# Kernel optimization log

Hardware: AMD Instinct MI355X
Metric: run time of the kernel (lower is better)

Reference implementation:

```python
import jax, jax.numpy as jnp
import numpy as np
import math

LOG_2PI = math.log(2.0 * math.pi)
MIN_CLIP, MAX_CLIP = -5.0, 5.0


def _lse(x, axis):
    return jax.nn.logsumexp(x, axis=axis)


def _gaussian_multi(m1, v1, m2, v2):
    # product of two diagonal Gaussians in log-std parameterization
    v1s = jnp.exp(2.0 * v1)
    v2s = jnp.exp(2.0 * v2)
    add = v1s + v2s
    la = jnp.log(add)
    scale = (-0.5 * (LOG_2PI + la + (m1 - m2) ** 2 / add)).sum(-1)
    mu = (m1 * v2s + m2 * v1s) / add
    var = v1 + v2 - 0.5 * la
    return scale, mu, var


def _energy(sents, mask, tw, tpm, tpv, tcm, tcv, sw_tab, sm_tab, sv_tab):
    B, T = sents.shape
    L, _, TC = tw.shape
    G = tpm.shape[-1]
    EC = sw_tab.shape[1] // L
    clip = lambda x: jnp.clip(x, MIN_CLIP, MAX_CLIP)
    s_mu = clip(sm_tab[sents].reshape(B, T, 1, L, 1, EC, G))
    s_var = clip(sv_tab[sents].reshape(B, T, 1, L, 1, EC, G))
    s_w = sw_tab[sents].reshape(B, T, 1, L, 1, EC)
    t_w = tw.reshape(1, 1, 1, L, L, 1, 1, TC)
    t_p_mu = clip(tpm.reshape(1, 1, 1, L, L, 1, 1, TC, G))
    t_p_var = clip(tpv.reshape(1, 1, 1, L, L, 1, 1, TC, G))
    t_c_mu = clip(tcm.reshape(1, 1, L, L, TC, 1, G))
    t_c_var = clip(tcv.reshape(1, 1, L, L, TC, 1, G))
    cs_scale, cs_mu, cs_var = _gaussian_multi(s_mu, s_var, t_c_mu, t_c_var)
    cs_scale = cs_scale + s_w  # (B,T,L,L,TC,EC)
    # parent-child fusion over consecutive timesteps -> (B,T-1,L,L,L,TC,EC,TC)
    csp, _, _ = _gaussian_multi(jnp.expand_dims(cs_mu[:, :-1], (4, 7)),
                                jnp.expand_dims(cs_var[:, :-1], (4, 7)),
                                t_p_mu, t_p_var)
    mask1 = mask[:, 1:].reshape(B, T - 1, 1, 1, 1, 1, 1, 1)
    csp = csp * mask1 + jnp.expand_dims(cs_scale[:, :-1], (4, 7)) + t_w * mask1
    last = jnp.broadcast_to(jnp.expand_dims(cs_scale[:, -1:], (4, 7)),
                            (B, 1, L, L, L, TC, EC, TC))
    energy = jnp.concatenate([csp, last], axis=1)
    return energy * mask.reshape(B, T, 1, 1, 1, 1, 1, 1)


def _loss(sents, target, mask, tw, tpm, tpv, tcm, tcv, sw_tab, sm_tab, sv_tab):
    B, T = sents.shape
    L, _, TC = tw.shape
    energy = _energy(sents, mask, tw, tpm, tpv, tcm, tcv, sw_tab, sm_tab, sv_tab)
    e_t = jnp.moveaxis(energy, 1, 0)  # (T,B,L,L,L,TC,EC,TC)
    tgt_t = target.T                  # (T,B)
    tgt_next = jnp.concatenate([tgt_t[1:], jnp.zeros((1, B), tgt_t.dtype)], axis=0)
    mask_t = mask.T                   # (T,B)
    bidx = jnp.arange(B)
    # t = 0 : root label is L-1
    e0 = e_t[0]
    part = _lse(_lse(e0[:, -1], axis=4), axis=3)  # (B,L,L,TC)
    tmp0 = e0[bidx, jnp.full((B,), L - 1), tgt_t[0], tgt_next[0]]  # (B,TC,EC,TC)
    tgt_e = _lse(_lse(tmp0, axis=2), axis=1)      # (B,TC) (initial tgt_energy is zeros)

    def step(carry, xs):
        part, tgt_e = carry
        e, tg, tn, pv, m = xs
        pn = _lse(_lse(_lse(e + part[:, :, :, None, :, None, None], 5), 4), 1)
        part = part + (pn - part) * m[:, None, None, None]
        tmp = e[bidx, pv, tg, tn]  # (B,TC,EC,TC)
        te_new = _lse(_lse(tmp + tgt_e[:, :, None, None], 2), 1)
        tgt_e = tgt_e + (te_new - tgt_e) * m[:, None]
        return (part, tgt_e), None

    (part, tgt_e), _ = jax.lax.scan(
        step, (part, tgt_e),
        (e_t[1:], tgt_t[1:], tgt_next[1:], tgt_t[:-1], mask_t[1:]))
    part = part.mean(axis=2)  # (B,L,TC)
    loss = _lse(_lse(part, 2), 1) - _lse(tgt_e, 1)
    return loss.mean()


def setup_inputs() -> dict:
    key = jax.random.key(0)
    ks = jax.random.split(key, 10)
    V, NL, G, TC, EC = 50000, 45, 1, 1, 1
    L = NL + 1
    B, T = 4, 96

    def xavier(k, shape):
        rf = int(np.prod(shape[2:])) if len(shape) > 2 else 1
        fan_in = shape[1] * rf
        fan_out = shape[0] * rf
        std = math.sqrt(2.0 / (fan_in + fan_out))
        return jax.random.normal(k, shape, jnp.float32) * std

    return {
        "sents": jax.random.randint(ks[0], (B, T), 0, V, dtype=jnp.int32),
        "target": jax.random.randint(ks[1], (B, T), 0, NL, dtype=jnp.int32),
        "mask": jnp.ones((B, T), jnp.float32),
        "trans_weight": xavier(ks[2], (L, L, TC)),
        "trans_p_mu": xavier(ks[3], (L, L, TC, G)),
        "trans_p_var": xavier(ks[4], (L, L, TC, G)),
        "trans_c_mu": xavier(ks[5], (L, L, TC, G)),
        "trans_c_var": xavier(ks[6], (L, L, TC, G)),
        "s_weight_tab": jax.random.normal(ks[7], (V, L * EC), jnp.float32),
        "s_mu_tab": jax.random.normal(ks[8], (V, L * G * EC), jnp.float32),
        "s_var_tab": jax.random.normal(ks[9], (V, L * G * EC), jnp.float32),
    }


def reference(sents, target, mask, trans_weight, trans_p_mu, trans_p_var,
              trans_c_mu, trans_c_var, s_weight_tab, s_mu_tab, s_var_tab):
    return _loss(sents, target, mask, trans_weight, trans_p_mu, trans_p_var,
                 trans_c_mu, trans_c_var, s_weight_tab, s_mu_tab, s_var_tab)
```

## Files before the change

kernel.cpp:

```cpp
#include <hip/hip_runtime.h>
#include <hip/hip_fp16.h>
#include <math.h>

#define L 46
#define LSQ 2116
#define T 96
#define B 4
#define WROWF 52
#define KSTRIDE_U32 25600
#define LOG_2PI 1.8378770664093453f
#define LN2f 0.6931471805599453f

typedef float v2f __attribute__((ext_vector_type(2)));

__device__ __forceinline__ float clip5(float x) {
    return fminf(fmaxf(x, -5.0f), 5.0f);
}

__device__ __forceinline__ unsigned fxform(float f) {
    unsigned u = __float_as_uint(f);
    return (u & 0x80000000u) ? ~u : (u | 0x80000000u);
}
__device__ __forceinline__ float funxform(unsigned u) {
    return __uint_as_float((u & 0x80000000u) ? (u ^ 0x80000000u) : ~u);
}

#define BARRIER_LGKM() asm volatile("s_waitcnt lgkmcnt(0)\n\ts_barrier" ::: "memory")

__device__ __forceinline__ unsigned enc_e4m3_sw(float f) {
    if (!(f >= 0.0f)) return 0u;
    if (f < 0.015625f) {
        int m = (int)rintf(f * 512.0f);
        return (unsigned)m;
    }
    unsigned u = __float_as_uint(fminf(f, 448.0f));
    int e = (int)((u >> 23) & 255) - 127;
    int mant = (int)((u >> 20) & 7) + (int)((u >> 19) & 1);
    int Eb = e + 7;
    if (mant == 8) { mant = 0; ++Eb; }
    if (Eb > 15) { Eb = 15; mant = 6; }
    return (unsigned)((Eb << 3) | mant);
}
template <bool HI>
__device__ __forceinline__ unsigned enc_pk(float a, float b, unsigned old) {
#if __has_builtin(__builtin_amdgcn_cvt_pk_fp8_f32)
    return (unsigned)__builtin_amdgcn_cvt_pk_fp8_f32(a, b, (int)old, HI);
#else
    unsigned lo = enc_e4m3_sw(a) | (enc_e4m3_sw(b) << 8);
    return HI ? ((old & 0x0000FFFFu) | (lo << 16)) : ((old & 0xFFFF0000u) | lo);
#endif
}

__device__ __forceinline__ float dec1_sw(unsigned b) {
    int e = (b >> 3) & 15, m = b & 7;
    return e ? ldexpf((float)(8 + m), e - 10) : ldexpf((float)m, -9);
}
template <bool HI>
__device__ __forceinline__ v2f dec_pk(unsigned u) {
#if __has_builtin(__builtin_amdgcn_cvt_pk_f32_fp8)
    return __builtin_amdgcn_cvt_pk_f32_fp8(u, HI);
#else
    unsigned x = HI ? (u >> 16) : u;
    v2f r; r.x = dec1_sw(x & 0xffu); r.y = dec1_sw((x >> 8) & 0xffu);
    return r;
#endif
}

__device__ __forceinline__ void dp_acc(v2f& acc, unsigned kv, v2f wA, v2f wB) {
    acc += dec_pk<false>(kv) * wA;
    acc += dec_pk<true>(kv)  * wB;
}

__global__ __launch_bounds__(1024) void build_kernel(
    const int*   __restrict__ sents,
    const int*   __restrict__ target,
    const float* __restrict__ tw,
    const float* __restrict__ tpm,
    const float* __restrict__ tpv,
    const float* __restrict__ tcm,
    const float* __restrict__ tcv,
    const float* __restrict__ sw_tab,
    const float* __restrict__ sm_tab,
    const float* __restrict__ sv_tab,
    unsigned* __restrict__ K8,
    float*    __restrict__ escB,
    float*    __restrict__ psD,
    float*    __restrict__ P0,
    float*    __restrict__ tgtc,
    unsigned* __restrict__ done)
{
    __shared__ float sPS[LSQ], sMU[LSQ], sW1[LSQ], sW2[LSQ], sTP[LSQ];
    const int bt = blockIdx.x;
    const int t  = bt % T;
    const int b  = bt / T;
    const int sent = sents[bt];

    if (bt == 0 && threadIdx.x == 0) *done = 0u;

    for (int i = threadIdx.x; i < LSQ; i += 1024) {
        sW2[i] = __expf(2.0f * clip5(tpv[i]));
        sTP[i] = clip5(tpm[i]);
        int bb = i % L;
        float smu  = clip5(sm_tab[sent * L + bb]);
        float svar = clip5(sv_tab[sent * L + bb]);
        float sw   = sw_tab[sent * L + bb];
        float tc_m = clip5(tcm[i]);
        float tc_v = clip5(tcv[i]);
        float v1s = __expf(2.0f * svar);
        float v2s = __expf(2.0f * tc_v);
        float add = v1s + v2s;
        float inv = __builtin_amdgcn_rcpf(add);
        float la  = __logf(add);
        float d   = smu - tc_m;
        float psv = fmaf(-0.5f, LOG_2PI + la + d * d * inv, sw);
        sPS[i] = psv;
        psD[(size_t)bt * LSQ + i] = psv;
        sMU[i] = (smu * v2s + tc_m * v1s) * inv;
        sW1[i] = v1s * v2s * inv;
    }
    __syncthreads();

    if (threadIdx.x == 0) {
        const int* tg = target + b * T;
        float contrib;
        if (t == 0) {
            int i1 = 45 * L + tg[0], i2 = tg[0] * L + tg[1];
            float ad = sW1[i1] + sW2[i2];
            float d  = sMU[i1] - sTP[i2];
            contrib = sPS[i1] + tw[i2]
                    - 0.5f * (LOG_2PI + __logf(ad) + d * d * __builtin_amdgcn_rcpf(ad));
        } else if (t == T - 1) {
            contrib = sPS[tg[T - 2] * L + tg[T - 1]];
        } else {
            int i1 = tg[t - 1] * L + tg[t], i2 = tg[t] * L + tg[t + 1];
            float ad = sW1[i1] + sW2[i2];
            float d  = sMU[i1] - sTP[i2];
            contrib = sPS[i1] + tw[i2]
                    - 0.5f * (LOG_2PI + __logf(ad) + d * d * __builtin_amdgcn_rcpf(ad));
        }
        tgtc[bt] = contrib;
    }

    if (t == 0) {
        for (int oi = threadIdx.x; oi < LSQ; oi += 1024) {
            int bb = oi / L;
            int i1 = 45 * L + bb;
            float ad = sW1[i1] + sW2[oi];
            float d  = sMU[i1] - sTP[oi];
            P0[b * LSQ + oi] = sPS[i1] + tw[oi]
                - 0.5f * (LOG_2PI + __logf(ad) + d * d * __builtin_amdgcn_rcpf(ad));
        }
        return;
    }
    if (t == T - 1) return;

    unsigned* Kb = K8 + (size_t)bt * KSTRIDE_U32;
    for (int oi = threadIdx.x; oi < LSQ; oi += 1024) {
        int bb = oi / L;
        float w2 = sW2[oi], tp = sTP[oi];
        float mx = 0.0f;
        #pragma unroll 2
        for (int a = 0; a < L; ++a) {
            float ad = sW1[a * L + bb] + w2;
            float r  = __builtin_amdgcn_rsqf(ad);
            float d  = sMU[a * L + bb] - tp;
            mx = fmaxf(mx, r * __expf(-0.5f * d * d * r * r));
        }
        mx = fmaxf(mx, 1e-30f);
        int iex = (int)((__float_as_uint(mx) >> 23) & 255);
        float sc = __uint_as_float((unsigned)(261 - iex) << 23);
        uint4* dst = (uint4*)(Kb + (size_t)oi * 12);
        #pragma unroll
        for (int j = 0; j < 3; ++j) {
            unsigned un[4];
            #pragma unroll
            for (int q = 0; q < 4; ++q) {
                float kk[4];
                #pragma unroll
                for (int z = 0; z < 4; ++z) {
                    int a = 16 * j + 4 * q + z;
                    if (a < L) {
                        float ad = sW1[a * L + bb] + w2;
                        float r  = __builtin_amdgcn_rsqf(ad);
                        float d  = sMU[a * L + bb] - tp;
                        kk[z] = sc * r * __expf(-0.5f * d * d * r * r);
                    } else kk[z] = 0.0f;
                }
                unsigned u = enc_pk<false>(kk[0], kk[1], 0u);
                un[q] = enc_pk<true>(kk[2], kk[3], u);
            }
            dst[j] = make_uint4(un[0], un[1], un[2], un[3]);
        }
        escB[(size_t)bt * LSQ + oi] =
            (float)(iex - 134) * LN2f + tw[oi] - 0.5f * LOG_2PI;
    }
}


#define DP_STEP(tt, KC, K3C, KN, K3N) do {                                    \
    const int t_ = (tt);                                                      \
    const int sM_ = t_ & 3;                      \
    const int sW_ = (t_ + 3) & 3;              \
    const int sP_ = (t_ + 2) & 3;             \
    const int sZ_ = (t_ + 1) & 3;                  \
    float2 esc2 = ((const float2*)(escM + (size_t)t_ * LSQ))[o];              \
    float2 psD2 = ((const float2*)(psDM + (size_t)(t_ + 1) * LSQ))[o];        \
    float psd3_ = 0.f, e3_ = 0.f;                                             \
    if (has3) {                                                               \
        e3_   = escM[(size_t)t_ * LSQ + oi3];                                 \
        psd3_ = psDM[(size_t)(t_ + 1) * LSQ + oi3];                           \
    }                                                                         \
    if (t_ < T - 2) {                                                         \
        const uint4* kp_ = (const uint4*)(KM + (size_t)(t_ + 1) * KSTRIDE_U32 \
                                          + (unsigned)(2 * o) * 12u);         \
        _Pragma("unroll")                                                     \
        for (int i_ = 0; i_ < 6; ++i_) KN[i_] = kp_[i_];                      \
        if (has3) {                                                           \
            const uint4* k3p_ = (const uint4*)(KM                             \
                + (size_t)(t_ + 1) * KSTRIDE_U32 + (unsigned)oi3 * 12u);      \
            _Pragma("unroll")                                                 \
            for (int i_ = 0; i_ < 3; ++i_) K3N[i_] = k3p_[i_];                \
        }                                                                     \
    }                                                                         \
    const float* wb_ = wbufF[t_ & 1];                                         \
    float*       wn_ = wbufF[(t_ + 1) & 1];                                   \
    {                                                                         \
        const float4* wrow4 = (const float4*)&wb_[bbA * WROWF];               \
        const unsigned* kru = (const unsigned*)KC;                            \
        v2f acc0 = {0.f, 0.f}, acc1 = {0.f, 0.f};                             \
        _Pragma("unroll")                                                     \
        for (int j_ = 0; j_ < 12; ++j_) {                                     \
            float4 w4 = wrow4[j_];                                            \
            v2f wA; wA.x = w4.x; wA.y = w4.y;                                 \
            v2f wB; wB.x = w4.z; wB.y = w4.w;                                 \
            dp_acc(acc0, kru[j_],      wA, wB);                               \
            dp_acc(acc1, kru[12 + j_], wA, wB);                               \
        }                                                                     \
        float shc = funxform(shiftS[sP_][bbA]);                               \
        float p0n = shc + __logf(fmaxf(acc0.x + acc0.y, 1e-37f)) + esc2.x;    \
        float p1n = shc + __logf(fmaxf(acc1.x + acc1.y, 1e-37f)) + esc2.y;    \
        float gA = p0n + psD2.x, gB = p1n + psD2.y;                           \
        atomicMax(&shiftS[sM_][c0],     fxform(gA));                          \
        atomicMax(&shiftS[sM_][c0 + 1], fxform(gB));                          \
        float shw0 = funxform(shiftS[sW_][c0]);                               \
        float shw1 = funxform(shiftS[sW_][c0 + 1]);                           \
        wn_[c0 * WROWF + bbA]       = __expf(fminf(gA - shw0, 80.f));         \
        wn_[(c0 + 1) * WROWF + bbA] = __expf(fminf(gB - shw1, 80.f));         \
        if (has3) {                                                           \
            const float4* wr34 = (const float4*)&wb_[bb3 * WROWF];            \
            const unsigned* k3u = (const unsigned*)K3C;                       \
            v2f acc3 = {0.f, 0.f};                                            \
            _Pragma("unroll")                                                 \
            for (int j_ = 0; j_ < 12; ++j_) {                                 \
                float4 w4 = wr34[j_];                                         \
                v2f wA; wA.x = w4.x; wA.y = w4.y;                             \
                v2f wB; wB.x = w4.z; wB.y = w4.w;                             \
                dp_acc(acc3, k3u[j_], wA, wB);                                \
            }                                                                 \
            float sh3 = funxform(shiftS[sP_][bb3]);                           \
            float p3n = sh3 + __logf(fmaxf(acc3.x + acc3.y, 1e-37f)) + e3_;   \
            float g3 = p3n + psd3_;                                           \
            atomicMax(&shiftS[sM_][c3], fxform(g3));                          \
            wn_[c3 * WROWF + bb3] =                                           \
                __expf(fminf(g3 - funxform(shiftS[sW_][c3]), 80.f));          \
        }                                                                     \
        if (o < L) shiftS[sZ_][o] = 0u;                                       \
    }                                                                         \
    BARRIER_LGKM();                                                           \
} while (0)

__global__ __launch_bounds__(1024, 4) void dp_kernel(
    const unsigned* __restrict__ K8,
    const float*    __restrict__ escB,
    const float*    __restrict__ psD,
    const float*    __restrict__ P0,
    const float*    __restrict__ tgtc,
    float*    __restrict__ zbuf,
    unsigned* __restrict__ done,
    float*    __restrict__ out)
{
    __shared__ float    wbufF[2][L * WROWF];
    __shared__ unsigned shiftS[4][L];
    __shared__ unsigned sh_last;
    __shared__ float    wsum[16];

    const int b = blockIdx.x;
    const int o = threadIdx.x;
    const int btT = b * T;

    const int bbA = (2 * o) / L;
    const int c0  = (2 * o) % L;
    const bool has3 = (o < LSQ - 2048);
    const int oi3 = 2048 + o;
    const int bb3 = has3 ? oi3 / L : 0;
    const int c3  = has3 ? oi3 % L : 0;

    const unsigned* KM   = K8   + (size_t)btT * KSTRIDE_U32;
    const float*    escM = escB + (size_t)btT * LSQ;
    const float*    psDM = psD  + (size_t)btT * LSQ;

    {
        const float* p0   = P0 + b * LSQ;
        const float* psd1 = psDM + LSQ;
        float2 p01 = ((const float2*)p0)[o];
        float2 d1  = ((const float2*)psd1)[o];
        float p3v = 0.f, d3v = 0.f;
        if (has3) { p3v = p0[oi3]; d3v = psd1[oi3]; }
        if (o < L) {
            shiftS[0][o] = 0u; shiftS[1][o] = 0u;
            shiftS[2][o] = 0u; shiftS[3][o] = 0u;
            wbufF[0][o * WROWF + 46] = 0.0f; wbufF[0][o * WROWF + 47] = 0.0f;
            wbufF[1][o * WROWF + 46] = 0.0f; wbufF[1][o * WROWF + 47] = 0.0f;
        }
        __syncthreads();
        float g0 = p01.x + d1.x, g1 = p01.y + d1.y, g3 = p3v + d3v;
        atomicMax(&shiftS[0][c0],     fxform(g0));
        atomicMax(&shiftS[0][c0 + 1], fxform(g1));
        if (has3) atomicMax(&shiftS[0][c3], fxform(g3));
        __syncthreads();
        if (o < L) shiftS[3][o] = shiftS[0][o];
        wbufF[1][c0 * WROWF + bbA] =
            __expf(fminf(g0 - funxform(shiftS[0][c0]), 80.f));
        wbufF[1][(c0 + 1) * WROWF + bbA] =
            __expf(fminf(g1 - funxform(shiftS[0][c0 + 1]), 80.f));
        if (has3)
            wbufF[1][c3 * WROWF + bb3] =
                __expf(fminf(g3 - funxform(shiftS[0][c3]), 80.f));
    }

    uint4 kA[6], kB[6], k3A[3], k3B[3];
    {
        const uint4* kp = (const uint4*)(KM + (size_t)KSTRIDE_U32
                                         + (unsigned)(2 * o) * 12u);
        #pragma unroll
        for (int i = 0; i < 6; ++i) kA[i] = kp[i];
        if (has3) {
            const uint4* k3p = (const uint4*)(KM + (size_t)KSTRIDE_U32
                                              + (unsigned)oi3 * 12u);
            #pragma unroll
            for (int i = 0; i < 3; ++i) k3A[i] = k3p[i];
        }
    }
    BARRIER_LGKM();

    for (int t = 1; t < T - 1; t += 2) {
        DP_STEP(t,     kA, k3A, kB, k3B);
        DP_STEP(t + 1, kB, k3B, kA, k3A);
    }

    if (o < 64) {
        float pn = -INFINITY;
        if (o < L) {
            const float4* wr = (const float4*)&wbufF[1][o * WROWF];
            float s = 0.0f;
            #pragma unroll
            for (int j = 0; j < 12; ++j) {
                float4 v = wr[j];
                s += (v.x + v.y) + (v.z + v.w);
            }
            pn = funxform(shiftS[1][o]) + __logf(s);
        }
        float mz = pn;
        #pragma unroll
        for (int off = 32; off >= 1; off >>= 1)
            mz = fmaxf(mz, __shfl_xor(mz, off));
        float ez = (o < L) ? __expf(pn - mz) : 0.0f;
        #pragma unroll
        for (int off = 32; off >= 1; off >>= 1)
            ez += __shfl_xor(ez, off);
        if (o == 0) zbuf[b] = mz + __logf(ez);
    }

    if (o == 0) {
        __threadfence();
        unsigned old = atomicAdd(done, 1u);
        sh_last = (old == B - 1) ? 1u : 0u;
    }
    __syncthreads();
    if (sh_last) {
        float v = (o < B * T) ? tgtc[o] : 0.0f;
        #pragma unroll
        for (int off = 32; off >= 1; off >>= 1) v += __shfl_xor(v, off);
        if ((o & 63) == 0) wsum[o >> 6] = v;
        __syncthreads();
        if (o == 0) {
            float ts = 0.0f;
            #pragma unroll
            for (int i = 0; i < 16; ++i) ts += wsum[i];
            __threadfence();
            float zs = zbuf[0] + zbuf[1] + zbuf[2] + zbuf[3];
            out[0] = 0.25f * (zs - ts);
        }
    }
}

__global__ __launch_bounds__(256) void prep_kernel(
    const int*   __restrict__ sents,
    const float* __restrict__ tcm,
    const float* __restrict__ tcv,
    const float* __restrict__ sw_tab,
    const float* __restrict__ sm_tab,
    const float* __restrict__ sv_tab,
    float* __restrict__ p_scale,
    float* __restrict__ p_mu,
    float* __restrict__ p_w1s)
{
    int idx = blockIdx.x * 256 + threadIdx.x;
    if (idx >= B * T * LSQ) return;
    int bb = idx % L;
    int bt = idx / LSQ;
    int sent = sents[bt];
    float smu  = clip5(sm_tab[sent * L + bb]);
    float svar = clip5(sv_tab[sent * L + bb]);
    float sw   = sw_tab[sent * L + bb];
    int i2 = idx % LSQ;
    float tc_m = clip5(tcm[i2]);
    float tc_v = clip5(tcv[i2]);
    float v1s = __expf(2.0f * svar);
    float v2s = __expf(2.0f * tc_v);
    float add = v1s + v2s;
    float inv = __builtin_amdgcn_rcpf(add);
    float la  = __logf(add);
    float d   = smu - tc_m;
    p_scale[idx] = fmaf(-0.5f, LOG_2PI + la + d * d * inv, sw);
    p_mu[idx]    = (smu * v2s + tc_m * v1s) * inv;
    p_w1s[idx]   = v1s * v2s * inv;
}

__global__ __launch_bounds__(1024) void dp_mono_kernel(
    const int*   __restrict__ target,
    const float* __restrict__ tw_g,
    const float* __restrict__ tpm_g,
    const float* __restrict__ tpv_g,
    const float* __restrict__ p_scale,
    const float* __restrict__ p_mu,
    const float* __restrict__ p_w1s,
    float* __restrict__ loss_out)
{
    __shared__ float sh_w2s[LSQ];
    __shared__ float sh_tpm[LSQ];
    __shared__ float sh_tw [LSQ];
    __shared__ float sh_w1s[LSQ];
    __shared__ float sh_mu [LSQ];
    __shared__ float sh_gf [LSQ];
    __shared__ float sh_P  [LSQ];
    __shared__ float sh_shift[L];
    __shared__ float sh_pn[L];

    const int b   = blockIdx.x;
    const int tid = threadIdx.x;
    const float* ps = p_scale + (size_t)b * T * LSQ;
    const float* pm = p_mu    + (size_t)b * T * LSQ;
    const float* pw = p_w1s   + (size_t)b * T * LSQ;
    const int*   tg = target + b * T;

    for (int i = tid; i < LSQ; i += 1024) {
        sh_w2s[i] = __expf(2.0f * clip5(tpv_g[i]));
        sh_tpm[i] = clip5(tpm_g[i]);
        sh_tw[i]  = tw_g[i];
    }
    __syncthreads();
    for (int oo = tid; oo < LSQ; oo += 1024) {
        int bb = oo / L;
        float cs_s = ps[45 * L + bb];
        float cm   = pm[45 * L + bb];
        float lw   = pw[45 * L + bb];
        float add2 = lw + sh_w2s[oo];
        float d    = cm - sh_tpm[oo];
        sh_P[oo] = cs_s + sh_tw[oo]
            - 0.5f * (LOG_2PI + __logf(add2) + d * d * __builtin_amdgcn_rcpf(add2));
    }
    __syncthreads();
    float tgt_e = 0.0f;
    if (tid == 0) tgt_e = sh_P[tg[0] * L + tg[1]];

    for (int t = 1; t < T - 1; ++t) {
        const float* ps_t = ps + t * LSQ;
        const float* pm_t = pm + t * LSQ;
        const float* pw_t = pw + t * LSQ;
        for (int i = tid; i < LSQ; i += 1024) {
            sh_w1s[i] = pw_t[i];
            sh_mu[i]  = pm_t[i];
            sh_gf[i]  = ps_t[i] + sh_P[i];
        }
        __syncthreads();
        if (tid < L) {
            float m = -INFINITY;
            for (int a = 0; a < L; ++a) m = fmaxf(m, sh_gf[a * L + tid]);
            sh_shift[tid] = m;
        }
        __syncthreads();
        for (int i = tid; i < LSQ; i += 1024) sh_gf[i] -= sh_shift[i % L];
        __syncthreads();
        for (int oo = tid; oo < LSQ; oo += 1024) {
            int bb = oo / L;
            float w2 = sh_w2s[oo], tp = sh_tpm[oo], tww = sh_tw[oo];
            float s = 0.0f;
            for (int a = 0; a < L; ++a) {
                float add2 = sh_w1s[a * L + bb] + w2;
                float r  = __builtin_amdgcn_rsqf(add2);
                float d  = sh_mu[a * L + bb] - tp;
                float y  = fmaf(-0.5f * d * d, r * r, sh_gf[a * L + bb]);
                s = fmaf(r, __expf(y), s);
            }
            sh_P[oo] = sh_shift[bb] + __logf(s) + tww - 0.5f * LOG_2PI;
        }
        if (tid == 0) {
            int pv = tg[t - 1], tc = tg[t], tn = tg[t + 1];
            float add2 = sh_w1s[pv * L + tc] + sh_w2s[tc * L + tn];
            float d    = sh_mu[pv * L + tc] - sh_tpm[tc * L + tn];
            tgt_e += ps_t[pv * L + tc] + sh_tw[tc * L + tn]
                - 0.5f * (LOG_2PI + __logf(add2) + d * d * __builtin_amdgcn_rcpf(add2));
        }
        __syncthreads();
    }
    {
        const float* ps_t = ps + (T - 1) * LSQ;
        for (int i = tid; i < LSQ; i += 1024) sh_gf[i] = ps_t[i] + sh_P[i];
        __syncthreads();
        if (tid < L) {
            float m = -INFINITY;
            for (int a = 0; a < L; ++a) m = fmaxf(m, sh_gf[a * L + tid]);
            float s = 0.0f;
            for (int a = 0; a < L; ++a) s += __expf(sh_gf[a * L + tid] - m);
            sh_pn[tid] = m + __logf(s);
        }
        __syncthreads();
        if (tid == 0) {
            tgt_e += ps_t[tg[T - 2] * L + tg[T - 1]];
            float m = -INFINITY;
            for (int bb = 0; bb < L; ++bb) m = fmaxf(m, sh_pn[bb]);
            float s = 0.0f;
            for (int bb = 0; bb < L; ++bb) s += __expf(sh_pn[bb] - m);
            loss_out[b] = (m + __logf(s)) - tgt_e;
        }
    }
}

__global__ void final_mono_kernel(const float* __restrict__ loss_partial,
                                  float* __restrict__ out)
{
    if (threadIdx.x == 0 && blockIdx.x == 0) {
        out[0] = 0.25f * (loss_partial[0] + loss_partial[1] +
                          loss_partial[2] + loss_partial[3]);
    }
}

extern "C" void kernel_launch(void* const* d_in, const int* in_sizes, int n_in,
                              void* d_out, int out_size, void* d_ws, size_t ws_size,
                              hipStream_t stream) {
    (void)in_sizes; (void)n_in; (void)out_size;

    const int*   sents  = (const int*)  d_in[0];
    const int*   target = (const int*)  d_in[1];
    const float* tw     = (const float*)d_in[3];
    const float* tpm    = (const float*)d_in[4];
    const float* tpv    = (const float*)d_in[5];
    const float* tcm    = (const float*)d_in[6];
    const float* tcv    = (const float*)d_in[7];
    const float* sw_tab = (const float*)d_in[8];
    const float* sm_tab = (const float*)d_in[9];
    const float* sv_tab = (const float*)d_in[10];

    char* ws = (char*)d_ws;

    size_t offK  = 0;
    size_t szK   = (size_t)B * T * KSTRIDE_U32 * 4;
    size_t offES = offK + szK;
    size_t szES  = (size_t)B * T * LSQ * sizeof(float);
    size_t offPD = offES + szES;
    size_t szPD  = (size_t)B * T * LSQ * sizeof(float);
    size_t offP0 = offPD + szPD;
    size_t szP0  = (size_t)B * LSQ * sizeof(float);
    size_t offTG = offP0 + szP0;
    size_t szTG  = (size_t)B * T * sizeof(float);
    size_t offZ  = offTG + szTG;
    size_t offDN = offZ + B * sizeof(float);
    size_t needed = offDN + sizeof(unsigned);

    if (ws_size >= needed) {
        unsigned* K8   = (unsigned*)(ws + offK);
        float*    escB = (float*)   (ws + offES);
        float*    psD  = (float*)   (ws + offPD);
        float*    P0   = (float*)   (ws + offP0);
        float*    tgtc = (float*)   (ws + offTG);
        float*    zbuf = (float*)   (ws + offZ);
        unsigned* done = (unsigned*)(ws + offDN);

        build_kernel<<<B * T, 1024, 0, stream>>>(
            sents, target, tw, tpm, tpv, tcm, tcv, sw_tab, sm_tab, sv_tab,
            K8, escB, psD, P0, tgtc, done);
        dp_kernel<<<B, 1024, 0, stream>>>(
            K8, escB, psD, P0, tgtc, zbuf, done, (float*)d_out);
    } else {
        float* p_scale      = (float*)ws;
        float* p_mu         = p_scale + (size_t)B * T * LSQ;
        float* p_w1s        = p_mu    + (size_t)B * T * LSQ;
        float* loss_partial = p_w1s   + (size_t)B * T * LSQ;
        int n = B * T * LSQ;
        prep_kernel<<<(n + 255) / 256, 256, 0, stream>>>(
            sents, tcm, tcv, sw_tab, sm_tab, sv_tab, p_scale, p_mu, p_w1s);
        dp_mono_kernel<<<B, 1024, 0, stream>>>(
            target, tw, tpm, tpv, p_scale, p_mu, p_w1s, loss_partial);
        final_mono_kernel<<<1, 64, 0, stream>>>(loss_partial, (float*)d_out);
    }
}
```

Before: 395.7 us.

## Replace per-step log/exp with bit-trick log estimate and single-buffered K loads

Rewrites the DP step loop so it no longer takes a log of the accumulated sum and then exponentiates it again. The max-shift is now estimated from the float's exponent bits (a cheap log2 approximation), and the weight is written as the accumulator multiplied by exp(base - shift). The K registers are now single-buffered and reloaded after the compute instead of prefetched before it, and the launch-bounds occupancy hint is dropped. This removes transcendental work and register pressure but exposes global load latency at each barrier, and the approximate max could weaken numerical stability.

```diff
diff --git a/kernel.cpp b/kernel.cpp
--- a/kernel.cpp
+++ b/kernel.cpp
@@ -10,6 +10,7 @@
 #define KSTRIDE_U32 25600
 #define LOG_2PI 1.8378770664093453f
 #define LN2f 0.6931471805599453f
+#define LN2_EXP 8.2629582e-8f
 
 typedef float v2f __attribute__((ext_vector_type(2)));
 
@@ -197,79 +198,24 @@
 }
 
 
-#define DP_STEP(tt, KC, K3C, KN, K3N) do {                                    \
-    const int t_ = (tt);                                                      \
-    const int sM_ = t_ & 3;                      \
-    const int sW_ = (t_ + 3) & 3;              \
-    const int sP_ = (t_ + 2) & 3;             \
-    const int sZ_ = (t_ + 1) & 3;                  \
-    float2 esc2 = ((const float2*)(escM + (size_t)t_ * LSQ))[o];              \
-    float2 psD2 = ((const float2*)(psDM + (size_t)(t_ + 1) * LSQ))[o];        \
-    float psd3_ = 0.f, e3_ = 0.f;                                             \
-    if (has3) {                                                               \
-        e3_   = escM[(size_t)t_ * LSQ + oi3];                                 \
-        psd3_ = psDM[(size_t)(t_ + 1) * LSQ + oi3];                           \
-    }                                                                         \
-    if (t_ < T - 2) {                                                         \
-        const uint4* kp_ = (const uint4*)(KM + (size_t)(t_ + 1) * KSTRIDE_U32 \
-                                          + (unsigned)(2 * o) * 12u);         \
-        _Pragma("unroll")                                                     \
-        for (int i_ = 0; i_ < 6; ++i_) KN[i_] = kp_[i_];                      \
-        if (has3) {                                                           \
-            const uint4* k3p_ = (const uint4*)(KM                             \
-                + (size_t)(t_ + 1) * KSTRIDE_U32 + (unsigned)oi3 * 12u);      \
-            _Pragma("unroll")                                                 \
-            for (int i_ = 0; i_ < 3; ++i_) K3N[i_] = k3p_[i_];                \
-        }                                                                     \
-    }                                                                         \
-    const float* wb_ = wbufF[t_ & 1];                                         \
-    float*       wn_ = wbufF[(t_ + 1) & 1];                                   \
+#define DOT_J(j, u0, u1)                                                      \
     {                                                                         \
-        const float4* wrow4 = (const float4*)&wb_[bbA * WROWF];               \
-        const unsigned* kru = (const unsigned*)KC;                            \
-        v2f acc0 = {0.f, 0.f}, acc1 = {0.f, 0.f};                             \
-        _Pragma("unroll")                                                     \
-        for (int j_ = 0; j_ < 12; ++j_) {                                     \
-            float4 w4 = wrow4[j_];                                            \
-            v2f wA; wA.x = w4.x; wA.y = w4.y;                                 \
-            v2f wB; wB.x = w4.z; wB.y = w4.w;                                 \
-            dp_acc(acc0, kru[j_],      wA, wB);                               \
-            dp_acc(acc1, kru[12 + j_], wA, wB);                               \
-        }                                                                     \
-        float shc = funxform(shiftS[sP_][bbA]);                               \
-        float p0n = shc + __logf(fmaxf(acc0.x + acc0.y, 1e-37f)) + esc2.x;    \
-        float p1n = shc + __logf(fmaxf(acc1.x + acc1.y, 1e-37f)) + esc2.y;    \
-        float gA = p0n + psD2.x, gB = p1n + psD2.y;                           \
-        atomicMax(&shiftS[sM_][c0],     fxform(gA));                          \
-        atomicMax(&shiftS[sM_][c0 + 1], fxform(gB));                          \
-        float shw0 = funxform(shiftS[sW_][c0]);                               \
-        float shw1 = funxform(shiftS[sW_][c0 + 1]);                           \
-        wn_[c0 * WROWF + bbA]       = __expf(fminf(gA - shw0, 80.f));         \
-        wn_[(c0 + 1) * WROWF + bbA] = __expf(fminf(gB - shw1, 80.f));         \
-        if (has3) {                                                           \
-            const float4* wr34 = (const float4*)&wb_[bb3 * WROWF];            \
-            const unsigned* k3u = (const unsigned*)K3C;                       \
-            v2f acc3 = {0.f, 0.f};                                            \
-            _Pragma("unroll")                                                 \
-            for (int j_ = 0; j_ < 12; ++j_) {                                 \
-                float4 w4 = wr34[j_];                                         \
-                v2f wA; wA.x = w4.x; wA.y = w4.y;                             \
-                v2f wB; wB.x = w4.z; wB.y = w4.w;                             \
-                dp_acc(acc3, k3u[j_], wA, wB);                                \
-            }                                                                 \
-            float sh3 = funxform(shiftS[sP_][bb3]);                           \
-            float p3n = sh3 + __logf(fmaxf(acc3.x + acc3.y, 1e-37f)) + e3_;   \
-            float g3 = p3n + psd3_;                                           \
-            atomicMax(&shiftS[sM_][c3], fxform(g3));                          \
-            wn_[c3 * WROWF + bb3] =                                           \
-                __expf(fminf(g3 - funxform(shiftS[sW_][c3]), 80.f));          \
-        }                                                                     \
-        if (o < L) shiftS[sZ_][o] = 0u;                                       \
-    }                                                                         \
-    BARRIER_LGKM();                                                           \
-} while (0)
-
-__global__ __launch_bounds__(1024, 4) void dp_kernel(
+        float4 w4 = wrow4[j];                                                 \
+        v2f wA; wA.x = w4.x; wA.y = w4.y;                                     \
+        v2f wB; wB.x = w4.z; wB.y = w4.w;                                     \
+        dp_acc(acc0, (u0), wA, wB);                                           \
+        dp_acc(acc1, (u1), wA, wB);                                           \
+    }
+
+#define DOT3_J(j, u0)                                                         \
+    {                                                                         \
+        float4 w4 = wr34[j];                                                  \
+        v2f wA; wA.x = w4.x; wA.y = w4.y;                                     \
+        v2f wB; wB.x = w4.z; wB.y = w4.w;                                     \
+        dp_acc(acc3, (u0), wA, wB);                                           \
+    }
+
+__global__ __launch_bounds__(1024) void dp_kernel(
     const unsigned* __restrict__ K8,
     const float*    __restrict__ escB,
     const float*    __restrict__ psD,
@@ -328,24 +274,98 @@
                 __expf(fminf(g3 - funxform(shiftS[0][c3]), 80.f));
     }
 
-    uint4 kA[6], kB[6], k3A[3], k3B[3];
+    uint4 k0, k1, k2, k3, k4, k5;
+    uint4 e0, e1, e2;
+    e0 = e1 = e2 = make_uint4(0u, 0u, 0u, 0u);
+
+    const unsigned kOffMain = (unsigned)(2 * o) * 12u;
+    const unsigned kOffExt  = (unsigned)oi3 * 12u;
+
     {
-        const uint4* kp = (const uint4*)(KM + (size_t)KSTRIDE_U32
-                                         + (unsigned)(2 * o) * 12u);
-        #pragma unroll
-        for (int i = 0; i < 6; ++i) kA[i] = kp[i];
+        const uint4* kp = (const uint4*)(KM + (size_t)KSTRIDE_U32 + kOffMain);
+        k0 = kp[0]; k1 = kp[1]; k2 = kp[2]; k3 = kp[3]; k4 = kp[4]; k5 = kp[5];
         if (has3) {
-            const uint4* k3p = (const uint4*)(KM + (size_t)KSTRIDE_U32
-                                              + (unsigned)oi3 * 12u);
-            #pragma unroll
-            for (int i = 0; i < 3; ++i) k3A[i] = k3p[i];
+            const uint4* ep = (const uint4*)(KM + (size_t)KSTRIDE_U32 + kOffExt);
+            e0 = ep[0]; e1 = ep[1]; e2 = ep[2];
         }
     }
     BARRIER_LGKM();
 
-    for (int t = 1; t < T - 1; t += 2) {
-        DP_STEP(t,     kA, k3A, kB, k3B);
-        DP_STEP(t + 1, kB, k3B, kA, k3A);
+    for (int t = 1; t < T - 1; ++t) {
+        const int sM_ = t & 3;
+        const int sW_ = (t + 3) & 3;
+        const int sP_ = (t + 2) & 3;
+        const int sZ_ = (t + 1) & 3;
+
+        float2 esc2 = ((const float2*)(escM + (size_t)t * LSQ))[o];
+        float2 psD2 = ((const float2*)(psDM + (size_t)(t + 1) * LSQ))[o];
+        float psd3_ = 0.f, e3_ = 0.f;
+        if (has3) {
+            e3_   = escM[(size_t)t * LSQ + oi3];
+            psd3_ = psDM[(size_t)(t + 1) * LSQ + oi3];
+        }
+
+        const float* wb_ = wbufF[t & 1];
+        float*       wn_ = wbufF[(t + 1) & 1];
+
+        const float4* wrow4 = (const float4*)&wb_[bbA * WROWF];
+        v2f acc0 = {0.f, 0.f}, acc1 = {0.f, 0.f};
+        DOT_J(0,  k0.x, k3.x) DOT_J(1,  k0.y, k3.y)
+        DOT_J(2,  k0.z, k3.z) DOT_J(3,  k0.w, k3.w)
+        DOT_J(4,  k1.x, k4.x) DOT_J(5,  k1.y, k4.y)
+        DOT_J(6,  k1.z, k4.z) DOT_J(7,  k1.w, k4.w)
+        DOT_J(8,  k2.x, k5.x) DOT_J(9,  k2.y, k5.y)
+        DOT_J(10, k2.z, k5.z) DOT_J(11, k2.w, k5.w)
+
+        v2f acc3 = {0.f, 0.f};
+        if (has3) {
+            const float4* wr34 = (const float4*)&wb_[bb3 * WROWF];
+            DOT3_J(0,  e0.x) DOT3_J(1,  e0.y) DOT3_J(2,  e0.z) DOT3_J(3,  e0.w)
+            DOT3_J(4,  e1.x) DOT3_J(5,  e1.y) DOT3_J(6,  e1.z) DOT3_J(7,  e1.w)
+            DOT3_J(8,  e2.x) DOT3_J(9,  e2.y) DOT3_J(10, e2.z) DOT3_J(11, e2.w)
+        }
+
+        {
+            float shc  = funxform(shiftS[sP_][bbA]);
+            float shw0 = funxform(shiftS[sW_][c0]);
+            float shw1 = funxform(shiftS[sW_][c0 + 1]);
+            float a0 = fmaxf(acc0.x + acc0.y, 1e-30f);
+            float a1 = fmaxf(acc1.x + acc1.y, 1e-30f);
+            float base0 = shc + esc2.x + psD2.x;
+            float base1 = shc + esc2.y + psD2.y;
+            float ga0 = fmaf((float)(int)(__float_as_uint(a0) - 0x3f800000u),
+                             LN2_EXP, base0);
+            float ga1 = fmaf((float)(int)(__float_as_uint(a1) - 0x3f800000u),
+                             LN2_EXP, base1);
+            atomicMax(&shiftS[sM_][c0],     fxform(ga0));
+            atomicMax(&shiftS[sM_][c0 + 1], fxform(ga1));
+            wn_[c0 * WROWF + bbA]       = a0 * __expf(fminf(base0 - shw0, 87.f));
+            wn_[(c0 + 1) * WROWF + bbA] = a1 * __expf(fminf(base1 - shw1, 87.f));
+            if (has3) {
+                float a3 = fmaxf(acc3.x + acc3.y, 1e-30f);
+                float sh3 = funxform(shiftS[sP_][bb3]);
+                float base3 = sh3 + e3_ + psd3_;
+                float ga3 = fmaf((float)(int)(__float_as_uint(a3) - 0x3f800000u),
+                                 LN2_EXP, base3);
+                atomicMax(&shiftS[sM_][c3], fxform(ga3));
+                wn_[c3 * WROWF + bb3] = a3 *
+                    __expf(fminf(base3 - funxform(shiftS[sW_][c3]), 87.f));
+            }
+            if (o < L) shiftS[sZ_][o] = 0u;
+        }
+
+        if (t < T - 2) {
+            const uint4* kp = (const uint4*)(KM + (size_t)(t + 1) * KSTRIDE_U32
+                                             + kOffMain);
+            k0 = kp[0]; k1 = kp[1]; k2 = kp[2];
+            k3 = kp[3]; k4 = kp[4]; k5 = kp[5];
+            if (has3) {
+                const uint4* ep = (const uint4*)(KM
+                    + (size_t)(t + 1) * KSTRIDE_U32 + kOffExt);
+                e0 = ep[0]; e1 = ep[1]; e2 = ep[2];
+            }
+        }
+        BARRIER_LGKM();
     }
 
     if (o < 64) {
```

Result: faster. 349.9 us (-11.6%).
